# Kernel tuning notes

Hardware: AMD Instinct MI355X
Metric: run time of the kernel (lower is better)

## Reference

```python
import jax, jax.numpy as jnp
import numpy as np

B, T, D, H = 32, 512, 512, 512


def _run_dir(x, W, b, reverse):
    # W: [D+H, 4H] packed gate weights in order [i, f, o, g]; b: [4H]
    Wx, Wh = W[:D], W[D:]
    # Precompute input contribution to all gates for all timesteps at once.
    xp = jnp.einsum('btd,dk->btk', x, Wx) + b  # [B, T, 4H]

    def step(carry, xt):
        h, c = carry
        z = xt + h @ Wh  # [B, 4H]
        i_t, f_t, o_t, g_t = jnp.split(z, 4, axis=-1)
        c = jax.nn.sigmoid(f_t) * c + jax.nn.sigmoid(i_t) * jnp.tanh(g_t)
        h = jax.nn.sigmoid(o_t) * jnp.tanh(c)
        return (h, c), h

    init = (jnp.zeros((x.shape[0], H), x.dtype), jnp.zeros((x.shape[0], H), x.dtype))
    _, hs = jax.lax.scan(step, init, xp.swapaxes(0, 1), reverse=reverse)  # [T, B, H]
    return hs.swapaxes(0, 1)  # [B, T, H]


def setup_inputs() -> dict:
    key = jax.random.key(0)
    ks = jax.random.split(key, 5)
    s_w = 1.0 / np.sqrt(D + H)
    x = jax.random.normal(ks[0], (B, T, D), dtype=jnp.float32)
    W_fw = jax.random.normal(ks[1], (D + H, 4 * H), dtype=jnp.float32) * s_w
    b_fw = jax.random.normal(ks[2], (4 * H,), dtype=jnp.float32) * s_w
    W_bw = jax.random.normal(ks[3], (D + H, 4 * H), dtype=jnp.float32) * s_w
    b_bw = jax.random.normal(ks[4], (4 * H,), dtype=jnp.float32) * s_w
    return {"x": x, "W_fw": W_fw, "b_fw": b_fw, "W_bw": W_bw, "b_bw": b_bw}


def reference(x, W_fw, b_fw, W_bw, b_bw):
    h_fw = _run_dir(x, W_fw, b_fw, reverse=False)
    h_bw = _run_dir(x, W_bw, b_bw, reverse=True)
    return jnp.concatenate([h_fw, h_bw], axis=-1)  # [B, T, 2H]
```

## Files before the change

kernel.cpp:

```cpp
#include <hip/hip_runtime.h>
#include <hip/hip_bf16.h>

#define Bz 32
#define Tz 512
#define Dz 512
#define Hz 512
#define NG 4
#define GWG 32
#define ROWS 16
#define COLS 16

typedef __attribute__((ext_vector_type(8))) short short8;
typedef __attribute__((ext_vector_type(4))) short short4v;
typedef __attribute__((ext_vector_type(4))) float f32x4;

#define HBUF (ROWS * Hz * 2)
#define WS_CNT 0
#define WS_H   512
#define WS_X   (512 + NG * 2 * HBUF)
#define WS_NEED ((size_t)WS_X + (size_t)Bz * Tz * Dz * 2)

__device__ __forceinline__ unsigned short f2bf(float f) {
    return __builtin_bit_cast(unsigned short, __float2bfloat16(f));
}
__device__ __forceinline__ float rcp_(float x) { return __builtin_amdgcn_rcpf(x); }
__device__ __forceinline__ float fsig(float x) { return rcp_(1.0f + __expf(-x)); }
__device__ __forceinline__ float ftanh(float x) {
    float t = __expf(-2.0f * fabsf(x));
    return copysignf((1.0f - t) * rcp_(1.0f + t), x);
}
__device__ __forceinline__ short8 mk8(unsigned long long lo, unsigned long long hi) {
    short4v a = __builtin_bit_cast(short4v, lo);
    short4v b = __builtin_bit_cast(short4v, hi);
    short8 r;
    r[0]=a[0]; r[1]=a[1]; r[2]=a[2]; r[3]=a[3];
    r[4]=b[0]; r[5]=b[1]; r[6]=b[2]; r[7]=b[3];
    return r;
}

__global__ void init_kernel(const float* __restrict__ x, unsigned char* __restrict__ ws, int do_x) {
    int tid = blockIdx.x * blockDim.x + threadIdx.x;
    unsigned int* w32 = (unsigned int*)ws;
    if (tid < (WS_X / 4)) w32[tid] = 0u;
    if (do_x) {
        const int n4 = (Bz * Tz * Dz) / 4;
        if (tid < n4) {
            const float4* xin = (const float4*)x;
            float4 v = xin[tid];
            unsigned int u0 = (unsigned)f2bf(v.x) | ((unsigned)f2bf(v.y) << 16);
            unsigned int u1 = (unsigned)f2bf(v.z) | ((unsigned)f2bf(v.w) << 16);
            unsigned int* xo = (unsigned int*)(ws + WS_X);
            xo[tid * 2]     = u0;
            xo[tid * 2 + 1] = u1;
        }
    }
}

template <bool XB>
__launch_bounds__(256, 1)
__global__ void lstm_kernel(const float* __restrict__ xf,
                            const float* __restrict__ Wf, const float* __restrict__ bf,
                            const float* __restrict__ Wb, const float* __restrict__ bb,
                            float* __restrict__ out, unsigned char* __restrict__ ws) {
    const int bi   = blockIdx.x;
    const int dir  = bi & 1;
    const int grp  = (bi >> 1) & 1;
    const int wg   = bi >> 2;
    const int gid  = dir * 2 + grp;
    const int j0   = wg * COLS;
    const int b0   = grp * ROWS;
    const int tid  = threadIdx.x;
    const int wave = tid >> 6;
    const int lane = tid & 63;
    const int nidx = lane & 15;
    const int quad = lane >> 4;

    const float* W    = dir ? Wb : Wf;
    const float* bias = dir ? bb : bf;

    unsigned int* cnt = (unsigned int*)(ws + WS_CNT + gid * 128);
    unsigned char* hbase = ws + WS_H + gid * 2 * HBUF;
    const unsigned short* xbf = (const unsigned short*)(ws + WS_X);

    __shared__ float part[4][4][16][17];

    short8 bfrag[8][4];
    {
        const int krow0 = (wave < 2) ? wave * 256 : 512 + (wave - 2) * 256;
        #pragma unroll
        for (int i = 0; i < 8; ++i) {
            #pragma unroll
            for (int g = 0; g < 4; ++g) {
                short8 v;
                #pragma unroll
                for (int jj = 0; jj < 8; ++jj) {
                    int krow = krow0 + i * 32 + quad * 8 + jj;
                    v[jj] = (short)f2bf(W[krow * (4 * Hz) + g * 512 + j0 + nidx]);
                }
                bfrag[i][g] = v;
            }
        }
    }

    const int erow = tid >> 4;
    const int ecol = tid & 15;
    float bia[4];
    #pragma unroll
    for (int g = 0; g < 4; ++g) bia[g] = bias[g * 512 + j0 + ecol];
    float creg = 0.f;
    const size_t outbase = ((size_t)(b0 + erow) * Tz) * (2 * Hz) + dir * Hz + j0 + ecol;

    int par = 0;
    for (int s = 0; s < Tz; ++s) {
        const int t = dir ? (Tz - 1 - s) : s;
        f32x4 acc[4] = {{0,0,0,0},{0,0,0,0},{0,0,0,0},{0,0,0,0}};

        if (wave < 2) {
            const int kb = wave * 256;
            short8 a[8];
            if (XB) {
                #pragma unroll
                for (int i = 0; i < 8; ++i) {
                    int k = kb + i * 32 + quad * 8;
                    a[i] = *(const short8*)(xbf + (((b0 + nidx) * Tz + t) * Dz + k));
                }
            } else {
                #pragma unroll
                for (int i = 0; i < 8; ++i) {
                    int k = kb + i * 32 + quad * 8;
                    const float* q = xf + (((b0 + nidx) * Tz + t) * Dz + k);
                    short8 sv;
                    #pragma unroll
                    for (int jj = 0; jj < 8; ++jj) sv[jj] = (short)f2bf(q[jj]);
                    a[i] = sv;
                }
            }
            #pragma unroll
            for (int i = 0; i < 8; ++i)
                #pragma unroll
                for (int g = 0; g < 4; ++g)
                    acc[g] = __builtin_amdgcn_mfma_f32_16x16x32_bf16(a[i], bfrag[i][g], acc[g], 0, 0, 0);
        } else {
            const unsigned target = (unsigned)(GWG * s);
            while (__hip_atomic_load(cnt, __ATOMIC_RELAXED, __HIP_MEMORY_SCOPE_AGENT) < target)
                __builtin_amdgcn_s_sleep(1);
            asm volatile("" ::: "memory");
            const unsigned long long* hb = (const unsigned long long*)(hbase + par * HBUF);
            const int kb = (wave - 2) * 256;
            short8 a[8];
            #pragma unroll
            for (int i = 0; i < 8; ++i) {
                int k  = kb + i * 32 + quad * 8;
                int i0 = (nidx * Hz + k) >> 2;
                unsigned long long l0 = __hip_atomic_load(hb + i0,     __ATOMIC_RELAXED, __HIP_MEMORY_SCOPE_AGENT);
                unsigned long long l1 = __hip_atomic_load(hb + i0 + 1, __ATOMIC_RELAXED, __HIP_MEMORY_SCOPE_AGENT);
                a[i] = mk8(l0, l1);
            }
            #pragma unroll
            for (int i = 0; i < 8; ++i)
                #pragma unroll
                for (int g = 0; g < 4; ++g)
                    acc[g] = __builtin_amdgcn_mfma_f32_16x16x32_bf16(a[i], bfrag[i][g], acc[g], 0, 0, 0);
        }

        {
            const int r0 = quad * 4;
            #pragma unroll
            for (int g = 0; g < 4; ++g)
                #pragma unroll
                for (int r = 0; r < 4; ++r)
                    part[wave][g][r0 + r][nidx] = acc[g][r];
        }
        __syncthreads();

        float hv;
        {
            float z[4];
            #pragma unroll
            for (int g = 0; g < 4; ++g)
                z[g] = bia[g] + part[0][g][erow][ecol] + part[1][g][erow][ecol]
                             + part[2][g][erow][ecol] + part[3][g][erow][ecol];
            float c = fsig(z[1]) * creg + fsig(z[0]) * ftanh(z[3]);
            creg = c;
            hv = fsig(z[2]) * ftanh(c);
            unsigned short* hw = (unsigned short*)(hbase + (par ^ 1) * HBUF);
            __hip_atomic_store(hw + erow * Hz + j0 + ecol, f2bf(hv),
                               __ATOMIC_RELAXED, __HIP_MEMORY_SCOPE_AGENT);
        }

        asm volatile("s_waitcnt vmcnt(0)" ::: "memory");
        __syncthreads();
        if (tid == 0)
            __hip_atomic_fetch_add(cnt, 1u, __ATOMIC_RELAXED, __HIP_MEMORY_SCOPE_AGENT);
        out[outbase + (size_t)t * (2 * Hz)] = hv;
        par ^= 1;
    }
}

extern "C" void kernel_launch(void* const* d_in, const int* in_sizes, int n_in,
                              void* d_out, int out_size, void* d_ws, size_t ws_size,
                              hipStream_t stream) {
    const float* x  = (const float*)d_in[0];
    const float* Wf = (const float*)d_in[1];
    const float* bf = (const float*)d_in[2];
    const float* Wb = (const float*)d_in[3];
    const float* bb = (const float*)d_in[4];
    float* out = (float*)d_out;
    unsigned char* ws = (unsigned char*)d_ws;
    const bool xb = (ws_size >= WS_NEED);

    init_kernel<<<8192, 256, 0, stream>>>(x, ws, xb ? 1 : 0);
    if (xb)
        lstm_kernel<true><<<NG * GWG, 256, 0, stream>>>(x, Wf, bf, Wb, bb, out, ws);
    else
        lstm_kernel<false><<<NG * GWG, 256, 0, stream>>>(x, Wf, bf, Wb, bb, out, ws);
}
```

Baseline: 2.088 ms.

## Replace counter barrier with step-tagged h values for flag-free sync

Each published hidden-state pair of bf16 values is now stored as a 64-bit word tagged with its step number. Consumers poll the data directly until every tag matches, which removes the global atomic counter, the vmcnt wait and the separate flag round trip per step. The cost is twice the bytes per h load and a poll that re-reads the whole fragment, plus reliance on 64-bit stores being atomic.

```diff
diff --git a/kernel.cpp b/kernel.cpp
--- a/kernel.cpp
+++ b/kernel.cpp
@@ -14,10 +14,11 @@
 typedef __attribute__((ext_vector_type(4))) short short4v;
 typedef __attribute__((ext_vector_type(4))) float f32x4;
 
-#define HBUF (ROWS * Hz * 2)
-#define WS_CNT 0
-#define WS_H   512
-#define WS_X   (512 + NG * 2 * HBUF)
+#define PAIRS (Hz / 2)
+#define TPU   (ROWS * PAIRS)
+#define TPB   (TPU * 8)
+#define WS_TP 0
+#define WS_X  (NG * 2 * TPB)
 #define WS_NEED ((size_t)WS_X + (size_t)Bz * Tz * Dz * 2)
 
 __device__ __forceinline__ unsigned short f2bf(float f) {
@@ -78,8 +79,7 @@
     const float* W    = dir ? Wb : Wf;
     const float* bias = dir ? bb : bf;
 
-    unsigned int* cnt = (unsigned int*)(ws + WS_CNT + gid * 128);
-    unsigned char* hbase = ws + WS_H + gid * 2 * HBUF;
+    unsigned long long* tp = (unsigned long long*)(ws + WS_TP + gid * 2 * TPB);
     const unsigned short* xbf = (const unsigned short*)(ws + WS_X);
 
     __shared__ float part[4][4][16][17];
@@ -110,7 +110,6 @@
     float creg = 0.f;
     const size_t outbase = ((size_t)(b0 + erow) * Tz) * (2 * Hz) + dir * Hz + j0 + ecol;
 
-    int par = 0;
     for (int s = 0; s < Tz; ++s) {
         const int t = dir ? (Tz - 1 - s) : s;
         f32x4 acc[4] = {{0,0,0,0},{0,0,0,0},{0,0,0,0},{0,0,0,0}};
@@ -141,26 +140,37 @@
                 for (int g = 0; g < 4; ++g)
                     acc[g] = __builtin_amdgcn_mfma_f32_16x16x32_bf16(a[i], bfrag[i][g], acc[g], 0, 0, 0);
         } else {
-            const unsigned target = (unsigned)(GWG * s);
-            while (__hip_atomic_load(cnt, __ATOMIC_RELAXED, __HIP_MEMORY_SCOPE_AGENT) < target)
+            unsigned long long* tpr = tp + (s & 1) * TPU;
+            const unsigned tg = (unsigned)s;
+            const int pb0 = ((wave - 2) * 256) >> 1;
+            unsigned long long v[8][4];
+            for (;;) {
+                #pragma unroll
+                for (int i = 0; i < 8; ++i) {
+                    int p = nidx * PAIRS + pb0 + i * 16 + quad * 4;
+                    #pragma unroll
+                    for (int jq = 0; jq < 4; ++jq)
+                        v[i][jq] = __hip_atomic_load(tpr + p + jq,
+                                                     __ATOMIC_RELAXED, __HIP_MEMORY_SCOPE_AGENT);
+                }
+                int ok = 1;
+                #pragma unroll
+                for (int i = 0; i < 8; ++i)
+                    #pragma unroll
+                    for (int jq = 0; jq < 4; ++jq)
+                        ok &= ((unsigned)v[i][jq] == tg);
+                if (__ballot(ok) == ~0ull) break;
                 __builtin_amdgcn_s_sleep(1);
-            asm volatile("" ::: "memory");
-            const unsigned long long* hb = (const unsigned long long*)(hbase + par * HBUF);
-            const int kb = (wave - 2) * 256;
-            short8 a[8];
+            }
             #pragma unroll
             for (int i = 0; i < 8; ++i) {
-                int k  = kb + i * 32 + quad * 8;
-                int i0 = (nidx * Hz + k) >> 2;
-                unsigned long long l0 = __hip_atomic_load(hb + i0,     __ATOMIC_RELAXED, __HIP_MEMORY_SCOPE_AGENT);
-                unsigned long long l1 = __hip_atomic_load(hb + i0 + 1, __ATOMIC_RELAXED, __HIP_MEMORY_SCOPE_AGENT);
-                a[i] = mk8(l0, l1);
-            }
-            #pragma unroll
-            for (int i = 0; i < 8; ++i)
+                unsigned long long lo = (v[i][0] >> 32) | ((v[i][1] >> 32) << 32);
+                unsigned long long hi = (v[i][2] >> 32) | ((v[i][3] >> 32) << 32);
+                short8 a = mk8(lo, hi);
                 #pragma unroll
                 for (int g = 0; g < 4; ++g)
-                    acc[g] = __builtin_amdgcn_mfma_f32_16x16x32_bf16(a[i], bfrag[i][g], acc[g], 0, 0, 0);
+                    acc[g] = __builtin_amdgcn_mfma_f32_16x16x32_bf16(a, bfrag[i][g], acc[g], 0, 0, 0);
+            }
         }
 
         {
@@ -173,7 +183,6 @@
         }
         __syncthreads();
 
-        float hv;
         {
             float z[4];
             #pragma unroll
@@ -182,18 +191,19 @@
                              + part[2][g][erow][ecol] + part[3][g][erow][ecol];
             float c = fsig(z[1]) * creg + fsig(z[0]) * ftanh(z[3]);
             creg = c;
-            hv = fsig(z[2]) * ftanh(c);
-            unsigned short* hw = (unsigned short*)(hbase + (par ^ 1) * HBUF);
-            __hip_atomic_store(hw + erow * Hz + j0 + ecol, f2bf(hv),
-                               __ATOMIC_RELAXED, __HIP_MEMORY_SCOPE_AGENT);
-        }
-
-        asm volatile("s_waitcnt vmcnt(0)" ::: "memory");
+            float hv = fsig(z[2]) * ftanh(c);
+
+            float hp = __shfl_xor(hv, 1);
+            if ((ecol & 1) == 0) {
+                unsigned d = (unsigned)f2bf(hv) | ((unsigned)f2bf(hp) << 16);
+                unsigned long long val = ((unsigned long long)d << 32) | (unsigned)(s + 1);
+                unsigned long long* tpw = tp + ((s + 1) & 1) * TPU;
+                int p = erow * PAIRS + ((j0 + ecol) >> 1);
+                __hip_atomic_store(tpw + p, val, __ATOMIC_RELAXED, __HIP_MEMORY_SCOPE_AGENT);
+            }
+            out[outbase + (size_t)t * (2 * Hz)] = hv;
+        }
         __syncthreads();
-        if (tid == 0)
-            __hip_atomic_fetch_add(cnt, 1u, __ATOMIC_RELAXED, __HIP_MEMORY_SCOPE_AGENT);
-        out[outbase + (size_t)t * (2 * Hz)] = hv;
-        par ^= 1;
     }
 }
 
```

New measurement: 2.720 ms. 1.3x slower.

## Replace atomic counter barrier with per-workgroup flags and pack h stores

Applied to the files above, without the earlier changes.

The shared atomic fetch-add counter used for the per-step inter-workgroup barrier becomes an array of per-workgroup step flags. Waiters poll all 32 flags in parallel across lanes and combine them with a ballot, so arrivals no longer contend on one atomic address. The hidden-state write also packs two bf16 values into one 32-bit store via a lane shuffle, halving the number of atomic stores. This relies on flag stores being ordered after the h writes under relaxed semantics, with the existing vmcnt wait providing that ordering.

```diff
diff --git a/kernel.cpp b/kernel.cpp
--- a/kernel.cpp
+++ b/kernel.cpp
@@ -15,9 +15,10 @@
 typedef __attribute__((ext_vector_type(4))) float f32x4;
 
 #define HBUF (ROWS * Hz * 2)
-#define WS_CNT 0
-#define WS_H   512
-#define WS_X   (512 + NG * 2 * HBUF)
+#define FLGB 512
+#define WS_FLG 0
+#define WS_H   (NG * FLGB)
+#define WS_X   (WS_H + NG * 2 * HBUF)
 #define WS_NEED ((size_t)WS_X + (size_t)Bz * Tz * Dz * 2)
 
 __device__ __forceinline__ unsigned short f2bf(float f) {
@@ -78,7 +79,7 @@
     const float* W    = dir ? Wb : Wf;
     const float* bias = dir ? bb : bf;
 
-    unsigned int* cnt = (unsigned int*)(ws + WS_CNT + gid * 128);
+    unsigned int* flg = (unsigned int*)(ws + WS_FLG + gid * FLGB);
     unsigned char* hbase = ws + WS_H + gid * 2 * HBUF;
     const unsigned short* xbf = (const unsigned short*)(ws + WS_X);
 
@@ -141,10 +142,15 @@
                 for (int g = 0; g < 4; ++g)
                     acc[g] = __builtin_amdgcn_mfma_f32_16x16x32_bf16(a[i], bfrag[i][g], acc[g], 0, 0, 0);
         } else {
-            const unsigned target = (unsigned)(GWG * s);
-            while (__hip_atomic_load(cnt, __ATOMIC_RELAXED, __HIP_MEMORY_SCOPE_AGENT) < target)
-                __builtin_amdgcn_s_sleep(1);
-            asm volatile("" ::: "memory");
+            {
+                const unsigned tgt = (unsigned)s;
+                const int fi = (lane & 31) * 4;
+                for (;;) {
+                    unsigned f = __hip_atomic_load(flg + fi, __ATOMIC_RELAXED, __HIP_MEMORY_SCOPE_AGENT);
+                    if (__ballot(f >= tgt) == ~0ull) break;
+                    __builtin_amdgcn_s_sleep(1);
+                }
+            }
             const unsigned long long* hb = (const unsigned long long*)(hbase + par * HBUF);
             const int kb = (wave - 2) * 256;
             short8 a[8];
@@ -183,15 +189,20 @@
             float c = fsig(z[1]) * creg + fsig(z[0]) * ftanh(z[3]);
             creg = c;
             hv = fsig(z[2]) * ftanh(c);
-            unsigned short* hw = (unsigned short*)(hbase + (par ^ 1) * HBUF);
-            __hip_atomic_store(hw + erow * Hz + j0 + ecol, f2bf(hv),
-                               __ATOMIC_RELAXED, __HIP_MEMORY_SCOPE_AGENT);
+            float hp = __shfl_xor(hv, 1);
+            if ((ecol & 1) == 0) {
+                unsigned d = (unsigned)f2bf(hv) | ((unsigned)f2bf(hp) << 16);
+                unsigned* hw = (unsigned*)(hbase + (par ^ 1) * HBUF);
+                __hip_atomic_store(hw + erow * (Hz / 2) + ((j0 + ecol) >> 1), d,
+                                   __ATOMIC_RELAXED, __HIP_MEMORY_SCOPE_AGENT);
+            }
         }
 
         asm volatile("s_waitcnt vmcnt(0)" ::: "memory");
         __syncthreads();
         if (tid == 0)
-            __hip_atomic_fetch_add(cnt, 1u, __ATOMIC_RELAXED, __HIP_MEMORY_SCOPE_AGENT);
+            __hip_atomic_store(flg + wg * 4, (unsigned)(s + 1),
+                               __ATOMIC_RELAXED, __HIP_MEMORY_SCOPE_AGENT);
         out[outbase + (size_t)t * (2 * Hz)] = hv;
         par ^= 1;
     }
```

Measured after the change: 1.946 ms. 1.07x faster.

## Replace counter barrier with per-value step-tagged h exchange and prefetch x projection

Applied to the files above, without the earlier changes.

Removes the global per-group atomic counter and instead packs each bf16 h pair with its step number into one 64-bit word, so waves poll only the slices of h they need and consume them as they arrive. Each workgroup now owns 32 columns (16 workgroups per group), and every wave handles both an x and an h K-slice instead of splitting x and h work across waves. The x-projection for the next step is computed after the current step's h is published, which takes it off the recurrence critical path. This costs more weight registers per wave and more polling traffic, and the slice-by-slice polling adds divergence.

```diff
diff --git a/kernel.cpp b/kernel.cpp
--- a/kernel.cpp
+++ b/kernel.cpp
@@ -6,18 +6,17 @@
 #define Dz 512
 #define Hz 512
 #define NG 4
-#define GWG 32
+#define GWG 16
 #define ROWS 16
-#define COLS 16
+#define COLS 32
+#define NT 8
 
 typedef __attribute__((ext_vector_type(8))) short short8;
-typedef __attribute__((ext_vector_type(4))) short short4v;
 typedef __attribute__((ext_vector_type(4))) float f32x4;
 
-#define HBUF (ROWS * Hz * 2)
-#define WS_CNT 0
-#define WS_H   512
-#define WS_X   (512 + NG * 2 * HBUF)
+#define TPU 4096
+#define TPB (TPU * 8)
+#define WS_X  (NG * 2 * TPB)
 #define WS_NEED ((size_t)WS_X + (size_t)Bz * Tz * Dz * 2)
 
 __device__ __forceinline__ unsigned short f2bf(float f) {
@@ -28,14 +27,6 @@
 __device__ __forceinline__ float ftanh(float x) {
     float t = __expf(-2.0f * fabsf(x));
     return copysignf((1.0f - t) * rcp_(1.0f + t), x);
-}
-__device__ __forceinline__ short8 mk8(unsigned long long lo, unsigned long long hi) {
-    short4v a = __builtin_bit_cast(short4v, lo);
-    short4v b = __builtin_bit_cast(short4v, hi);
-    short8 r;
-    r[0]=a[0]; r[1]=a[1]; r[2]=a[2]; r[3]=a[3];
-    r[4]=b[0]; r[5]=b[1]; r[6]=b[2]; r[7]=b[3];
-    return r;
 }
 
 __global__ void init_kernel(const float* __restrict__ x, unsigned char* __restrict__ ws, int do_x) {
@@ -78,122 +69,142 @@
     const float* W    = dir ? Wb : Wf;
     const float* bias = dir ? bb : bf;
 
-    unsigned int* cnt = (unsigned int*)(ws + WS_CNT + gid * 128);
-    unsigned char* hbase = ws + WS_H + gid * 2 * HBUF;
+    unsigned long long* tp = (unsigned long long*)(ws + (size_t)gid * 2 * TPB);
     const unsigned short* xbf = (const unsigned short*)(ws + WS_X);
 
-    __shared__ float part[4][4][16][17];
-
-    short8 bfrag[8][4];
-    {
-        const int krow0 = (wave < 2) ? wave * 256 : 512 + (wave - 2) * 256;
+    __shared__ float part[4][NT][16][18];
+
+    short8 bx[4][NT], bh[4][NT];
+    const int w4 = wave * 4;
+    #pragma unroll
+    for (int i = 0; i < 4; ++i) {
+        const int k0 = 32 * (w4 + i) + quad * 8;
         #pragma unroll
-        for (int i = 0; i < 8; ++i) {
-            #pragma unroll
-            for (int g = 0; g < 4; ++g) {
-                short8 v;
-                #pragma unroll
-                for (int jj = 0; jj < 8; ++jj) {
-                    int krow = krow0 + i * 32 + quad * 8 + jj;
-                    v[jj] = (short)f2bf(W[krow * (4 * Hz) + g * 512 + j0 + nidx]);
+        for (int nt = 0; nt < NT; ++nt) {
+            const int col = (nt >> 1) * 512 + j0 + (nt & 1) * 16 + nidx;
+            short8 vx, vh;
+            #pragma unroll
+            for (int jj = 0; jj < 8; ++jj) {
+                vx[jj] = (short)f2bf(W[(k0 + jj) * (4 * Hz) + col]);
+                vh[jj] = (short)f2bf(W[(512 + k0 + jj) * (4 * Hz) + col]);
+            }
+            bx[i][nt] = vx;
+            bh[i][nt] = vh;
+        }
+    }
+
+    const int erow = tid >> 4;
+    const int e    = tid & 15;
+    const int c0   = 2 * e;
+    const int ci   = c0 & 15;
+    const int nt0  = c0 >> 4;
+    float bia[4][2];
+    #pragma unroll
+    for (int g = 0; g < 4; ++g) {
+        bia[g][0] = bias[g * 512 + j0 + c0];
+        bia[g][1] = bias[g * 512 + j0 + c0 + 1];
+    }
+    float cr0 = 0.f, cr1 = 0.f;
+    float* outp = out + ((size_t)(b0 + erow) * Tz) * (2 * Hz) + dir * Hz + j0 + c0;
+
+    f32x4 acc[NT];
+    auto xpart = [&](int t) {
+        #pragma unroll
+        for (int nt = 0; nt < NT; ++nt) acc[nt] = (f32x4){0.f, 0.f, 0.f, 0.f};
+        #pragma unroll
+        for (int i = 0; i < 4; ++i) {
+            const int k = 32 * (w4 + i) + quad * 8;
+            short8 ax;
+            if (XB) {
+                ax = *(const short8*)(xbf + ((size_t)(b0 + nidx) * Tz + t) * Dz + k);
+            } else {
+                const float* q = xf + ((size_t)(b0 + nidx) * Tz + t) * Dz + k;
+                #pragma unroll
+                for (int jj = 0; jj < 8; ++jj) ax[jj] = (short)f2bf(q[jj]);
+            }
+            #pragma unroll
+            for (int nt = 0; nt < NT; ++nt)
+                acc[nt] = __builtin_amdgcn_mfma_f32_16x16x32_bf16(ax, bx[i][nt], acc[nt], 0, 0, 0);
+        }
+    };
+
+    xpart(dir ? (Tz - 1) : 0);
+
+    for (int s = 0; s < Tz; ++s) {
+        {
+            const unsigned long long* tpr = tp + (size_t)(s & 1) * TPU;
+            const unsigned tg = (unsigned)s;
+            unsigned rm = 0;
+            while (rm != 0xFu) {
+                bool prog = false;
+                #pragma unroll
+                for (int i = 0; i < 4; ++i) if (!((rm >> i) & 1u)) {
+                    const unsigned long long* bp = tpr + (((w4 + i) * 16 + nidx) * 16 + quad * 4);
+                    unsigned long long v0 = __hip_atomic_load(bp + 0, __ATOMIC_RELAXED, __HIP_MEMORY_SCOPE_AGENT);
+                    unsigned long long v1 = __hip_atomic_load(bp + 1, __ATOMIC_RELAXED, __HIP_MEMORY_SCOPE_AGENT);
+                    unsigned long long v2 = __hip_atomic_load(bp + 2, __ATOMIC_RELAXED, __HIP_MEMORY_SCOPE_AGENT);
+                    unsigned long long v3 = __hip_atomic_load(bp + 3, __ATOMIC_RELAXED, __HIP_MEMORY_SCOPE_AGENT);
+                    int ok = ((unsigned)v0 == tg) & ((unsigned)v1 == tg) &
+                             ((unsigned)v2 == tg) & ((unsigned)v3 == tg);
+                    if (__ballot(ok) == ~0ull) {
+                        unsigned h0 = (unsigned)(v0 >> 32), h1 = (unsigned)(v1 >> 32);
+                        unsigned h2 = (unsigned)(v2 >> 32), h3 = (unsigned)(v3 >> 32);
+                        short8 a;
+                        a[0] = (short)h0; a[1] = (short)(h0 >> 16);
+                        a[2] = (short)h1; a[3] = (short)(h1 >> 16);
+                        a[4] = (short)h2; a[5] = (short)(h2 >> 16);
+                        a[6] = (short)h3; a[7] = (short)(h3 >> 16);
+                        #pragma unroll
+                        for (int nt = 0; nt < NT; ++nt)
+                            acc[nt] = __builtin_amdgcn_mfma_f32_16x16x32_bf16(a, bh[i][nt], acc[nt], 0, 0, 0);
+                        rm |= 1u << i;
+                        prog = true;
+                    }
                 }
-                bfrag[i][g] = v;
-            }
-        }
-    }
-
-    const int erow = tid >> 4;
-    const int ecol = tid & 15;
-    float bia[4];
-    #pragma unroll
-    for (int g = 0; g < 4; ++g) bia[g] = bias[g * 512 + j0 + ecol];
-    float creg = 0.f;
-    const size_t outbase = ((size_t)(b0 + erow) * Tz) * (2 * Hz) + dir * Hz + j0 + ecol;
-
-    int par = 0;
-    for (int s = 0; s < Tz; ++s) {
-        const int t = dir ? (Tz - 1 - s) : s;
-        f32x4 acc[4] = {{0,0,0,0},{0,0,0,0},{0,0,0,0},{0,0,0,0}};
-
-        if (wave < 2) {
-            const int kb = wave * 256;
-            short8 a[8];
-            if (XB) {
-                #pragma unroll
-                for (int i = 0; i < 8; ++i) {
-                    int k = kb + i * 32 + quad * 8;
-                    a[i] = *(const short8*)(xbf + (((b0 + nidx) * Tz + t) * Dz + k));
-                }
-            } else {
-                #pragma unroll
-                for (int i = 0; i < 8; ++i) {
-                    int k = kb + i * 32 + quad * 8;
-                    const float* q = xf + (((b0 + nidx) * Tz + t) * Dz + k);
-                    short8 sv;
-                    #pragma unroll
-                    for (int jj = 0; jj < 8; ++jj) sv[jj] = (short)f2bf(q[jj]);
-                    a[i] = sv;
-                }
-            }
-            #pragma unroll
-            for (int i = 0; i < 8; ++i)
-                #pragma unroll
-                for (int g = 0; g < 4; ++g)
-                    acc[g] = __builtin_amdgcn_mfma_f32_16x16x32_bf16(a[i], bfrag[i][g], acc[g], 0, 0, 0);
-        } else {
-            const unsigned target = (unsigned)(GWG * s);
-            while (__hip_atomic_load(cnt, __ATOMIC_RELAXED, __HIP_MEMORY_SCOPE_AGENT) < target)
-                __builtin_amdgcn_s_sleep(1);
-            asm volatile("" ::: "memory");
-            const unsigned long long* hb = (const unsigned long long*)(hbase + par * HBUF);
-            const int kb = (wave - 2) * 256;
-            short8 a[8];
-            #pragma unroll
-            for (int i = 0; i < 8; ++i) {
-                int k  = kb + i * 32 + quad * 8;
-                int i0 = (nidx * Hz + k) >> 2;
-                unsigned long long l0 = __hip_atomic_load(hb + i0,     __ATOMIC_RELAXED, __HIP_MEMORY_SCOPE_AGENT);
-                unsigned long long l1 = __hip_atomic_load(hb + i0 + 1, __ATOMIC_RELAXED, __HIP_MEMORY_SCOPE_AGENT);
-                a[i] = mk8(l0, l1);
-            }
-            #pragma unroll
-            for (int i = 0; i < 8; ++i)
-                #pragma unroll
-                for (int g = 0; g < 4; ++g)
-                    acc[g] = __builtin_amdgcn_mfma_f32_16x16x32_bf16(a[i], bfrag[i][g], acc[g], 0, 0, 0);
+                if (!prog && rm != 0xFu) __builtin_amdgcn_s_sleep(1);
+            }
         }
 
         {
             const int r0 = quad * 4;
             #pragma unroll
-            for (int g = 0; g < 4; ++g)
+            for (int nt = 0; nt < NT; ++nt)
                 #pragma unroll
                 for (int r = 0; r < 4; ++r)
-                    part[wave][g][r0 + r][nidx] = acc[g][r];
+                    part[wave][nt][r0 + r][nidx] = acc[nt][r];
         }
         __syncthreads();
 
-        float hv;
+        const int t = dir ? (Tz - 1 - s) : s;
         {
-            float z[4];
-            #pragma unroll
-            for (int g = 0; g < 4; ++g)
-                z[g] = bia[g] + part[0][g][erow][ecol] + part[1][g][erow][ecol]
-                             + part[2][g][erow][ecol] + part[3][g][erow][ecol];
-            float c = fsig(z[1]) * creg + fsig(z[0]) * ftanh(z[3]);
-            creg = c;
-            hv = fsig(z[2]) * ftanh(c);
-            unsigned short* hw = (unsigned short*)(hbase + (par ^ 1) * HBUF);
-            __hip_atomic_store(hw + erow * Hz + j0 + ecol, f2bf(hv),
-                               __ATOMIC_RELAXED, __HIP_MEMORY_SCOPE_AGENT);
-        }
-
-        asm volatile("s_waitcnt vmcnt(0)" ::: "memory");
+            float z[4][2];
+            #pragma unroll
+            for (int g = 0; g < 4; ++g) {
+                const int nt = g * 2 + nt0;
+                float sx = bia[g][0], sy = bia[g][1];
+                #pragma unroll
+                for (int w = 0; w < 4; ++w) {
+                    const float2 p = *(const float2*)&part[w][nt][erow][ci];
+                    sx += p.x; sy += p.y;
+                }
+                z[g][0] = sx; z[g][1] = sy;
+            }
+            float cA = fsig(z[1][0]) * cr0 + fsig(z[0][0]) * ftanh(z[3][0]); cr0 = cA;
+            float hA = fsig(z[2][0]) * ftanh(cA);
+            float cB = fsig(z[1][1]) * cr1 + fsig(z[0][1]) * ftanh(z[3][1]); cr1 = cB;
+            float hB = fsig(z[2][1]) * ftanh(cB);
+
+            unsigned pk = (unsigned)f2bf(hA) | ((unsigned)f2bf(hB) << 16);
+            unsigned long long val = ((unsigned long long)pk << 32) | (unsigned)(s + 1);
+            unsigned long long* tpw = tp + (size_t)((s + 1) & 1) * TPU + ((wg * 16 + erow) * 16 + e);
+            __hip_atomic_store(tpw, val, __ATOMIC_RELAXED, __HIP_MEMORY_SCOPE_AGENT);
+
+            float2 ov; ov.x = hA; ov.y = hB;
+            *(float2*)(outp + (size_t)t * (2 * Hz)) = ov;
+        }
         __syncthreads();
-        if (tid == 0)
-            __hip_atomic_fetch_add(cnt, 1u, __ATOMIC_RELAXED, __HIP_MEMORY_SCOPE_AGENT);
-        out[outbase + (size_t)t * (2 * Hz)] = hv;
-        par ^= 1;
+
+        if (s + 1 < Tz) xpart(dir ? (Tz - 2 - s) : (s + 1));
     }
 }
 
```

Result: no change. 2.089 ms (+0.1%).
